# Optimization experiments

Hardware: AMD Instinct MI355X
Metric: run time of the kernel (lower is better)

Reference implementation:

```python
import jax, jax.numpy as jnp
import numpy as np

NUM_HEADS = 16
LN_EPS = 1e-5


def _rope(x):
    """lucidrains RotaryEmbedding(dim_per_head // 2): rotate only the first
    Dh//2 channels with interleaved pairs; pass the rest through.
    x: (B, H, S, Dh)"""
    S, D = x.shape[-2], x.shape[-1]
    rot = D // 2
    inv_freq = 1.0 / (10000.0 ** (jnp.arange(0, rot, 2, dtype=jnp.float32) / rot))  # (rot//2,)
    ang = jnp.arange(S, dtype=jnp.float32)[:, None] * inv_freq[None, :]             # (S, rot//2)
    ang = jnp.repeat(ang, 2, axis=-1)                                               # (S, rot)
    cos, sin = jnp.cos(ang), jnp.sin(ang)
    xr, xp = x[..., :rot], x[..., rot:]
    x1, x2 = xr[..., 0::2], xr[..., 1::2]
    rot_half = jnp.stack((-x2, x1), axis=-1).reshape(xr.shape)  # interleaved (-x2, x1)
    xr = xr * cos + rot_half * sin
    return jnp.concatenate([xr, xp], axis=-1)


def setup_inputs() -> dict:
    key = jax.random.key(0)
    k1, k2, k3 = jax.random.split(key, 3)
    B, S, D = 4, 2048, 2048
    X = jax.random.normal(k1, (B, S, D), dtype=jnp.float32)
    ln_w = jnp.ones((D,), dtype=jnp.float32)
    ln_b = jnp.zeros((D,), dtype=jnp.float32)
    W_in = jax.random.normal(k2, (D, 3 * D), dtype=jnp.float32) * 0.02
    W_out = jax.random.normal(k3, (D, D), dtype=jnp.float32) * 0.02
    return {"X": X, "ln_w": ln_w, "ln_b": ln_b, "W_in": W_in, "W_out": W_out}


def reference(X, ln_w, ln_b, W_in, W_out):
    B, S, D = X.shape
    H = NUM_HEADS
    Dh = D // H
    # pre-norm (LayerNorm)
    mu = jnp.mean(X, axis=-1, keepdims=True)
    var = jnp.mean(jnp.square(X - mu), axis=-1, keepdims=True)
    Xn = (X - mu) * jax.lax.rsqrt(var + LN_EPS) * ln_w + ln_b
    # fused QKV projection
    qkv = jnp.einsum('bsd,df->bsf', Xn, W_in)            # (B, S, 3D)
    Q, K, V = jnp.split(qkv, 3, axis=-1)
    Q = Q.reshape(B, S, H, Dh).transpose(0, 2, 1, 3)     # (B, H, S, Dh)
    K = K.reshape(B, S, H, Dh).transpose(0, 2, 1, 3)
    V = V.reshape(B, S, H, Dh).transpose(0, 2, 1, 3)
    Q, K = _rope(Q), _rope(K)
    scores = jnp.einsum('bhqd,bhkd->bhqk', Q, K) / jnp.sqrt(jnp.float32(Dh))
    probs = jax.nn.softmax(scores, axis=-1)              # acausal: no mask
    ctx = jnp.einsum('bhqk,bhkd->bhqd', probs, V)
    ctx = ctx.transpose(0, 2, 1, 3).reshape(B, S, D)
    out = jnp.einsum('bsd,df->bsf', ctx, W_out)
    return out + X
```

## Files before the change

### kernel.cpp

```cpp
#include <hip/hip_runtime.h>
#include <hip/hip_bf16.h>
#include <cstddef>

#define B_ 4
#define S_ 2048
#define D_ 2048
#define H_ 16
#define DH_ 128
#define QKS_ 4096

typedef __attribute__((ext_vector_type(8))) short bfrag8;
typedef __attribute__((ext_vector_type(4))) float ffrag4;

typedef const __attribute__((address_space(1))) void* gptr1;
typedef __attribute__((address_space(3))) void* lptr3;
#define GL16(g, l) __builtin_amdgcn_global_load_lds((gptr1)(g), (lptr3)(l), 16, 0, 0)

#define BARRIER() { asm volatile("" ::: "memory"); __builtin_amdgcn_s_barrier(); asm volatile("" ::: "memory"); }
#define VMW8() asm volatile("s_waitcnt vmcnt(8)" ::: "memory")
#define VMW4() asm volatile("s_waitcnt vmcnt(4)" ::: "memory")
#define VMW0() asm volatile("s_waitcnt vmcnt(0)" ::: "memory")

__device__ __forceinline__ short f2bf(float f) {
  unsigned u = __float_as_uint(f);
  u = (u + 0x7FFFu + ((u >> 16) & 1u)) >> 16;
  return (short)u;
}
__device__ __forceinline__ float bf2f(short s) {
  return __uint_as_float(((unsigned)(unsigned short)s) << 16);
}
__device__ __forceinline__ unsigned pk2(float lo, float hi) {
  unsigned a = __float_as_uint(lo);
  a = (a + 0x7FFFu + ((a >> 16) & 1u)) >> 16;
  unsigned b = __float_as_uint(hi);
  b = (b + 0x7FFFu + ((b >> 16) & 1u)) & 0xFFFF0000u;
  return a | b;
}

__global__ __launch_bounds__(256) void rope_tab_kernel(float2* __restrict__ tab) {
  int idx = blockIdx.x * 256 + threadIdx.x;
  int s = idx >> 5, p = idx & 31;
  float invf = exp2f(-(float)p * (13.287712379549449f / 32.0f));
  float sn, cs;
  sincosf((float)s * invf, &sn, &cs);
  tab[idx] = make_float2(cs, sn);
}

__global__ __launch_bounds__(256) void ln_kernel(const float* __restrict__ X,
    const float* __restrict__ w, const float* __restrict__ bta,
    short* __restrict__ Xn) {
  int row = blockIdx.x;
  int tid = threadIdx.x;
  const float* xr = X + (size_t)row * D_;
  float x[8];
  float4 v0 = *(const float4*)(xr + tid * 4);
  float4 v1 = *(const float4*)(xr + 1024 + tid * 4);
  x[0] = v0.x; x[1] = v0.y; x[2] = v0.z; x[3] = v0.w;
  x[4] = v1.x; x[5] = v1.y; x[6] = v1.z; x[7] = v1.w;
  float sum = 0.f, ssq = 0.f;
#pragma unroll
  for (int i = 0; i < 8; i++) { sum += x[i]; ssq += x[i] * x[i]; }
#pragma unroll
  for (int off = 1; off < 64; off <<= 1) {
    sum += __shfl_xor(sum, off, 64);
    ssq += __shfl_xor(ssq, off, 64);
  }
  __shared__ float s1[4], s2[4];
  int wave = tid >> 6;
  if ((tid & 63) == 0) { s1[wave] = sum; s2[wave] = ssq; }
  __syncthreads();
  sum = s1[0] + s1[1] + s1[2] + s1[3];
  ssq = s2[0] + s2[1] + s2[2] + s2[3];
  float mu = sum * (1.0f / D_);
  float var = ssq * (1.0f / D_) - mu * mu;
  float rs = rsqrtf(var + 1e-5f);
  short* orow = Xn + (size_t)row * D_;
#pragma unroll
  for (int i = 0; i < 8; i++) {
    int col = (i < 4) ? (tid * 4 + i) : (1024 + tid * 4 + (i - 4));
    float xn = (x[i] - mu) * rs * w[col] + bta[col];
    orow[col] = f2bf(xn);
  }
}

__global__ __launch_bounds__(256) void transpose_cvt(const float* __restrict__ W,
    short* __restrict__ WT, int R, int C) {
  __shared__ float t[32][33];
  int tx = threadIdx.x, ty = threadIdx.y;
  int c0 = blockIdx.x * 32, r0 = blockIdx.y * 32;
#pragma unroll
  for (int i = 0; i < 4; i++)
    t[ty + i * 8][tx] = W[(size_t)(r0 + ty + i * 8) * C + c0 + tx];
  __syncthreads();
#pragma unroll
  for (int i = 0; i < 4; i++)
    WT[(size_t)(c0 + ty + i * 8) * R + r0 + tx] = f2bf(t[tx][ty + i * 8]);
}

template<int EPI>
__global__ __launch_bounds__(512) void gemm_bt(const short* __restrict__ A,
    const short* __restrict__ Bt, short* __restrict__ Cb, short* __restrict__ Vt,
    const float2* __restrict__ tab, float* __restrict__ Cf,
    const float* __restrict__ resid, int M, int N, int K) {
  __shared__ __align__(16) short lA[2][2][256][32];
  __shared__ __align__(16) short lB[2][2][256][32];
  int tid = threadIdx.x;
  int wave = tid >> 6, lane = tid & 63;
  int m16 = lane & 15, quad = lane >> 4;
  int wm = (wave >> 2) * 128, wn = (wave & 3) * 64;

  int bid = blockIdx.x;
  int q = bid & 7, c = bid >> 3;
  int xb = c >> 2;
  int yb = (q << 2) | (c & 3);
  int m0 = yb * 256, n0 = xb * 256;

  const ffrag4 fzero = {0.f, 0.f, 0.f, 0.f};
  ffrag4 acc[8][4];
#pragma unroll
  for (int i = 0; i < 8; i++)
#pragma unroll
    for (int j = 0; j < 4; j++) acc[i][j] = fzero;

  int r0_ = tid >> 2;
  int csw = ((tid & 3) ^ ((r0_ >> 1) & 3)) << 3;
  const short* gA0 = A + (size_t)(m0 + r0_) * K + csw;
  const short* gA1 = A + (size_t)(m0 + r0_ + 128) * K + csw;
  const short* gB0 = Bt + (size_t)(n0 + r0_) * K + csw;
  const short* gB1 = Bt + (size_t)(n0 + r0_ + 128) * K + csw;
  int ldW = wave << 10;

#define STG(g0, g1, larr, kt, h, d) { \
    const short* s0_ = (g0) + ((size_t)(kt) << 6) + ((h) << 5); \
    const short* s1_ = (g1) + ((size_t)(kt) << 6) + ((h) << 5); \
    char* dst_ = (char*)(larr) + (((d) << 15) | ((h) << 14)) + ldW; \
    GL16(s0_, dst_); \
    GL16(s1_, dst_ + 8192); }

  int offA[8], offB[4];
#pragma unroll
  for (int mi = 0; mi < 8; mi++) {
    int ra = wm + mi * 16 + m16;
    offA[mi] = ra * 64 + ((quad ^ ((ra >> 1) & 3)) << 4);
  }
#pragma unroll
  for (int ni = 0; ni < 4; ni++) {
    int rb = wn + ni * 16 + m16;
    offB[ni] = rb * 64 + ((quad ^ ((rb >> 1) & 3)) << 4);
  }
  const char* cA = (const char*)lA;
  const char* cB = (const char*)lB;

  STG(gA0, gA1, lA, 0, 0, 0); STG(gB0, gB1, lB, 0, 0, 0);
  STG(gA0, gA1, lA, 0, 1, 0); STG(gB0, gB1, lB, 0, 1, 0);
  STG(gA0, gA1, lA, 1, 0, 1); STG(gB0, gB1, lB, 1, 0, 1);
  VMW8();
  BARRIER();

  int nK = K >> 6;
  for (int t = 0; t < nK; ++t) {
    int cur = t & 1, nxt = cur ^ 1;
    int s1 = (t + 1 < nK), s2 = (t + 2 < nK);
    int h0 = cur << 15;
    int h1 = h0 | 16384;
    bfrag8 bf[4], af[4];

#pragma unroll
    for (int ni = 0; ni < 4; ni++) bf[ni] = *(const bfrag8*)(cB + h0 + offB[ni]);
#pragma unroll
    for (int mi = 0; mi < 4; mi++) af[mi] = *(const bfrag8*)(cA + h0 + offA[mi]);
    if (s1) STG(gA0, gA1, lA, t + 1, 1, nxt);
    BARRIER();
    __builtin_amdgcn_s_setprio(1);
#pragma unroll
    for (int mi = 0; mi < 4; mi++)
#pragma unroll
      for (int ni = 0; ni < 4; ni++)
        acc[mi][ni] = __builtin_amdgcn_mfma_f32_16x16x32_bf16(af[mi], bf[ni], acc[mi][ni], 0, 0, 0);
    __builtin_amdgcn_s_setprio(0);
    BARRIER();

#pragma unroll
    for (int mi = 0; mi < 4; mi++) af[mi] = *(const bfrag8*)(cA + h0 + offA[mi + 4]);
    if (s1) STG(gB0, gB1, lB, t + 1, 1, nxt);
    BARRIER();
    __builtin_amdgcn_s_setprio(1);
#pragma unroll
    for (int mi = 0; mi < 4; mi++)
#pragma unroll
      for (int ni = 0; ni < 4; ni++)
        acc[mi + 4][ni] = __builtin_amdgcn_mfma_f32_16x16x32_bf16(af[mi], bf[ni], acc[mi + 4][ni], 0, 0, 0);
    __builtin_amdgcn_s_setprio(0);
    if (s1) { VMW8(); } else { VMW0(); }
    BARRIER();

#pragma unroll
    for (int ni = 0; ni < 4; ni++) bf[ni] = *(const bfrag8*)(cB + h1 + offB[ni]);
#pragma unroll
    for (int mi = 0; mi < 4; mi++) af[mi] = *(const bfrag8*)(cA + h1 + offA[mi]);
    if (s2) STG(gA0, gA1, lA, t + 2, 0, cur);
    BARRIER();
    __builtin_amdgcn_s_setprio(1);
#pragma unroll
    for (int mi = 0; mi < 4; mi++)
#pragma unroll
      for (int ni = 0; ni < 4; ni++)
        acc[mi][ni] = __builtin_amdgcn_mfma_f32_16x16x32_bf16(af[mi], bf[ni], acc[mi][ni], 0, 0, 0);
    __builtin_amdgcn_s_setprio(0);
    BARRIER();

#pragma unroll
    for (int mi = 0; mi < 4; mi++) af[mi] = *(const bfrag8*)(cA + h1 + offA[mi + 4]);
    if (s2) STG(gB0, gB1, lB, t + 2, 0, cur);
    BARRIER();
    __builtin_amdgcn_s_setprio(1);
#pragma unroll
    for (int mi = 0; mi < 4; mi++)
#pragma unroll
      for (int ni = 0; ni < 4; ni++)
        acc[mi + 4][ni] = __builtin_amdgcn_mfma_f32_16x16x32_bf16(af[mi], bf[ni], acc[mi + 4][ni], 0, 0, 0);
    __builtin_amdgcn_s_setprio(0);
    if (s2) { VMW8(); } else if (s1) { VMW4(); }
    BARRIER();
  }
#undef STG

#pragma unroll
  for (int mi = 0; mi < 8; mi++) {
    int rowb = m0 + wm + mi * 16 + quad * 4;
#pragma unroll
    for (int ni = 0; ni < 4; ni++) {
      int col = n0 + wn + ni * 16 + m16;
      if (EPI == 1) {
#pragma unroll
        for (int r = 0; r < 4; r++) {
          size_t idx = (size_t)(rowb + r) * N + col;
          Cf[idx] = acc[mi][ni][r] + resid[idx];
        }
      } else if (n0 >= 4096) {
        int d = col - 4096;
        short4 pk;
        pk.x = f2bf(acc[mi][ni][0]);
        pk.y = f2bf(acc[mi][ni][1]);
        pk.z = f2bf(acc[mi][ni][2]);
        pk.w = f2bf(acc[mi][ni][3]);
        *(short4*)(Vt + ((size_t)((rowb >> 11) * H_ + (d >> 7)) * DH_ + (d & 127)) * S_ +
                   (rowb & (S_ - 1))) = pk;
      } else if ((col & 127) < 64) {
        int p = (col & 127) >> 1;
        float sgn = (col & 1) ? 1.0f : -1.0f;
#pragma unroll
        for (int r = 0; r < 4; r++) {
          float own = acc[mi][ni][r];
          float prt = __shfl_xor(own, 1, 64);
          float2 cssn = tab[((rowb + r) & (S_ - 1)) * 32 + p];
          Cb[(size_t)(rowb + r) * QKS_ + col] = f2bf(own * cssn.x + sgn * prt * cssn.y);
        }
      } else {
#pragma unroll
        for (int r = 0; r < 4; r++)
          Cb[(size_t)(rowb + r) * QKS_ + col] = f2bf(acc[mi][ni][r]);
      }
    }
  }
}

__global__ __launch_bounds__(512) void attn_kernel(const short* __restrict__ qkv,
    const short* __restrict__ Vt, short* __restrict__ ctx) {
  __shared__ __align__(16) short lK[2][64 * 128];
  __shared__ __align__(16) short lV[2][128 * 64];
  int tid = threadIdx.x;
  int wave = tid >> 6, lane = tid & 63;
  int m16 = lane & 15, quad = lane >> 4;
  int bh = blockIdx.y;
  int b = bh >> 4, h = bh & 15;
  int qbase = blockIdx.x * 256 + wave * 32;

  const float qscale = 1.4426950408889634f * 0.08838834764831845f;
  bfrag8 qf[2][4];
#pragma unroll
  for (int qb = 0; qb < 2; qb++)
#pragma unroll
    for (int kc = 0; kc < 4; kc++) {
      bfrag8 q = *(const bfrag8*)(qkv +
          (size_t)(b * S_ + qbase + qb * 16 + m16) * QKS_ + h * DH_ + kc * 32 + quad * 8);
#pragma unroll
      for (int j = 0; j < 8; j++) q[j] = f2bf(bf2f(q[j]) * qscale);
      qf[qb][kc] = q;
    }

  const ffrag4 fzero = {0.f, 0.f, 0.f, 0.f};
  ffrag4 oacc[2][8];
#pragma unroll
  for (int qb = 0; qb < 2; qb++)
#pragma unroll
    for (int nd = 0; nd < 8; nd++) oacc[qb][nd] = fzero;
  float lpart[2] = {0.f, 0.f};

  int krow = lane >> 4;
  int kcb = lane & 15;
  int vrow = lane >> 3;
  int vcb = lane & 7;

  {
#pragma unroll
    for (int i = 0; i < 2; i++) {
      int c = wave + i * 8;
      int r = c * 4 + krow;
      int sb = kcb ^ (r & 15);
      GL16(qkv + (size_t)(b * S_ + r) * QKS_ + D_ + h * DH_ + sb * 8, &lK[0][c * 512]);
    }
#pragma unroll
    for (int i = 0; i < 2; i++) {
      int c = wave + i * 8;
      int r = c * 8 + vrow;
      int sb = vcb ^ (r & 7);
      GL16(Vt + (size_t)(bh * DH_ + r) * S_ + sb * 8, &lV[0][c * 512]);
    }
  }
  __syncthreads();

  for (int kt = 0; kt < 32; kt++) {
    int cur = kt & 1;
    if (kt < 31) {
      int sk0 = (kt + 1) * 64;
      int nb = cur ^ 1;
#pragma unroll
      for (int i = 0; i < 2; i++) {
        int c = wave + i * 8;
        int r = c * 4 + krow;
        int sb = kcb ^ (r & 15);
        GL16(qkv + (size_t)(b * S_ + sk0 + r) * QKS_ + D_ + h * DH_ + sb * 8, &lK[nb][c * 512]);
      }
#pragma unroll
      for (int i = 0; i < 2; i++) {
        int c = wave + i * 8;
        int r = c * 8 + vrow;
        int sb = vcb ^ (r & 7);
        GL16(Vt + (size_t)(bh * DH_ + r) * S_ + sk0 + sb * 8, &lV[nb][c * 512]);
      }
    }

    const short* kb = &lK[cur][0];
    const short* vb = &lV[cur][0];

    ffrag4 sacc[2][4];
#pragma unroll
    for (int qb = 0; qb < 2; qb++)
#pragma unroll
      for (int ntk = 0; ntk < 4; ntk++) sacc[qb][ntk] = fzero;
#pragma unroll
    for (int ntk = 0; ntk < 4; ntk++)
#pragma unroll
      for (int kc = 0; kc < 4; kc++) {
        bfrag8 kf = *(const bfrag8*)(kb + (ntk * 16 + m16) * 128 +
                                     (((kc * 4 + quad) ^ m16) << 3));
        sacc[0][ntk] = __builtin_amdgcn_mfma_f32_16x16x32_bf16(kf, qf[0][kc], sacc[0][ntk], 0, 0, 0);
        sacc[1][ntk] = __builtin_amdgcn_mfma_f32_16x16x32_bf16(kf, qf[1][kc], sacc[1][ntk], 0, 0, 0);
      }

    bfrag8 pA[2][2];
#pragma unroll
    for (int qb = 0; qb < 2; qb++) {
      unsigned Xp[4][2];
      float ls = 0.f;
#pragma unroll
      for (int ntk = 0; ntk < 4; ntk++) {
        float e0 = exp2f(sacc[qb][ntk][0]);
        float e1 = exp2f(sacc[qb][ntk][1]);
        float e2 = exp2f(sacc[qb][ntk][2]);
        float e3 = exp2f(sacc[qb][ntk][3]);
        ls += (e0 + e1) + (e2 + e3);
        Xp[ntk][0] = pk2(e0, e1);
        Xp[ntk][1] = pk2(e2, e3);
      }
      lpart[qb] += ls;
#pragma unroll
      for (int kc = 0; kc < 2; kc++) {
        unsigned x0 = Xp[2 * kc][0], x1 = Xp[2 * kc][1];
        unsigned y0 = Xp[2 * kc + 1][0], y1 = Xp[2 * kc + 1][1];
        asm("v_permlane32_swap_b32 %0, %1" : "+v"(x0), "+v"(y0));
        asm("v_permlane16_swap_b32 %0, %1" : "+v"(x0), "+v"(y0));
        asm("v_permlane32_swap_b32 %0, %1" : "+v"(x1), "+v"(y1));
        asm("v_permlane16_swap_b32 %0, %1" : "+v"(x1), "+v"(y1));
        union { int4 i4; bfrag8 b8; } u;
        u.i4 = (int4){(int)x0, (int)x1, (int)y0, (int)y1};
        pA[qb][kc] = u.b8;
      }
    }

#pragma unroll
    for (int kc = 0; kc < 2; kc++)
#pragma unroll
      for (int nd = 0; nd < 8; nd++) {
        bfrag8 vf = *(const bfrag8*)(vb + (nd * 16 + m16) * 64 +
                                     (((kc * 4 + quad) ^ (m16 & 7)) << 3));
        oacc[0][nd] = __builtin_amdgcn_mfma_f32_16x16x32_bf16(pA[0][kc], vf, oacc[0][nd], 0, 0, 0);
        oacc[1][nd] = __builtin_amdgcn_mfma_f32_16x16x32_bf16(pA[1][kc], vf, oacc[1][nd], 0, 0, 0);
      }

    __syncthreads();
  }

#pragma unroll
  for (int qb = 0; qb < 2; qb++) {
    lpart[qb] += __shfl_xor(lpart[qb], 16, 64);
    lpart[qb] += __shfl_xor(lpart[qb], 32, 64);
  }
#pragma unroll
  for (int qb = 0; qb < 2; qb++) {
    float inv[4];
#pragma unroll
    for (int r = 0; r < 4; r++) inv[r] = 1.0f / __shfl(lpart[qb], quad * 4 + r, 64);
#pragma unroll
    for (int nd = 0; nd < 8; nd++)
#pragma unroll
      for (int r = 0; r < 4; r++) {
        int row = qbase + qb * 16 + quad * 4 + r;
        int col = h * DH_ + nd * 16 + m16;
        ctx[(size_t)(b * S_ + row) * D_ + col] = f2bf(oacc[qb][nd][r] * inv[r]);
      }
  }
}

extern "C" void kernel_launch(void* const* d_in, const int* in_sizes, int n_in,
                              void* d_out, int out_size, void* d_ws, size_t ws_size,
                              hipStream_t stream) {
  const float* X    = (const float*)d_in[0];
  const float* lnw  = (const float*)d_in[1];
  const float* lnb  = (const float*)d_in[2];
  const float* Win  = (const float*)d_in[3];
  const float* Wout = (const float*)d_in[4];
  float* out = (float*)d_out;
  char* ws = (char*)d_ws;
  short*  Xn    = (short*)(ws + 0);
  short*  WinT  = (short*)(ws + 33554432);
  short*  WoutT = (short*)(ws + 58720256);
  short*  qkv   = (short*)(ws + 67108864);
  short*  Vt    = (short*)(ws + 134217728);
  short*  ctx   = (short*)(ws + 167772160);
  float2* tab   = (float2*)(ws + 201326592);

  rope_tab_kernel<<<256, 256, 0, stream>>>(tab);
  transpose_cvt<<<dim3(192, 64), dim3(32, 8), 0, stream>>>(Win, WinT, 2048, 6144);
  transpose_cvt<<<dim3(64, 64), dim3(32, 8), 0, stream>>>(Wout, WoutT, 2048, 2048);
  ln_kernel<<<8192, 256, 0, stream>>>(X, lnw, lnb, Xn);
  gemm_bt<0><<<768, 512, 0, stream>>>(Xn, WinT, qkv, Vt, tab, nullptr, nullptr, 8192, 6144, 2048);
  attn_kernel<<<dim3(8, 64), 512, 0, stream>>>(qkv, Vt, ctx);
  gemm_bt<1><<<256, 512, 0, stream>>>(ctx, WoutT, nullptr, nullptr, nullptr, out, X, 8192, 2048, 2048);
}
```

Baseline: 647.2 us.

## Software-pipeline LDS fragment loads with MFMA via double-buffered register fragments

Restructures the GEMM K-loop so LDS reads for the next sub-tile are issued while MFMAs for the current sub-tile run. Fragments are ping-ponged between two register sets, barriers drop from eight to four per K-tile, and the loop is peeled so the tail iterations need no runtime conditionals. It also adds a launch-bounds occupancy hint of two blocks and retunes the vmcnt waits. The extra fragment registers raise register pressure, which could cause spills under the tighter occupancy bound, and the reworked wait counts must still cover the async global-to-LDS copies.

```diff
diff --git a/kernel.cpp b/kernel.cpp
--- a/kernel.cpp
+++ b/kernel.cpp
@@ -18,6 +18,7 @@
 
 #define BARRIER() { asm volatile("" ::: "memory"); __builtin_amdgcn_s_barrier(); asm volatile("" ::: "memory"); }
 #define VMW8() asm volatile("s_waitcnt vmcnt(8)" ::: "memory")
+#define VMW6() asm volatile("s_waitcnt vmcnt(6)" ::: "memory")
 #define VMW4() asm volatile("s_waitcnt vmcnt(4)" ::: "memory")
 #define VMW0() asm volatile("s_waitcnt vmcnt(0)" ::: "memory")
 
@@ -98,7 +99,7 @@
 }
 
 template<int EPI>
-__global__ __launch_bounds__(512) void gemm_bt(const short* __restrict__ A,
+__global__ __launch_bounds__(512, 2) void gemm_bt(const short* __restrict__ A,
     const short* __restrict__ Bt, short* __restrict__ Cb, short* __restrict__ Vt,
     const float2* __restrict__ tab, float* __restrict__ Cf,
     const float* __restrict__ resid, int M, int N, int K) {
@@ -151,78 +152,89 @@
   const char* cA = (const char*)lA;
   const char* cB = (const char*)lB;
 
+  bfrag8 afA[4], afB[4], bfA[4], bfB[4];
+
+#define MF16(AF, BF, BASE) { \
+    __builtin_amdgcn_s_setprio(1); \
+    _Pragma("unroll") \
+    for (int mi_ = 0; mi_ < 4; mi_++) \
+      _Pragma("unroll") \
+      for (int ni_ = 0; ni_ < 4; ni_++) \
+        acc[(BASE) + mi_][ni_] = __builtin_amdgcn_mfma_f32_16x16x32_bf16( \
+            AF[mi_], BF[ni_], acc[(BASE) + mi_][ni_], 0, 0, 0); \
+    __builtin_amdgcn_s_setprio(0); }
+
+#define KTILE(T, S1, S2) { \
+    const int cur_ = (T) & 1, nxt_ = cur_ ^ 1; \
+    const int h0_ = cur_ << 15; \
+    const int h1_ = h0_ | 16384; \
+    const int g0_ = nxt_ << 15; \
+     \
+    BARRIER(); \
+    afB[0] = *(const bfrag8*)(cA + h0_ + offA[4]); \
+    afB[1] = *(const bfrag8*)(cA + h0_ + offA[5]); \
+    afB[2] = *(const bfrag8*)(cA + h0_ + offA[6]); \
+    afB[3] = *(const bfrag8*)(cA + h0_ + offA[7]); \
+    if (S1) STG(gA0, gA1, lA, (T) + 1, 1, nxt_); \
+    MF16(afA, bfA, 0); \
+    if (S1) { VMW6(); } else { VMW0(); } \
+     \
+    BARRIER(); \
+    bfB[0] = *(const bfrag8*)(cB + h1_ + offB[0]); \
+    bfB[1] = *(const bfrag8*)(cB + h1_ + offB[1]); \
+    bfB[2] = *(const bfrag8*)(cB + h1_ + offB[2]); \
+    bfB[3] = *(const bfrag8*)(cB + h1_ + offB[3]); \
+    afA[0] = *(const bfrag8*)(cA + h1_ + offA[0]); \
+    afA[1] = *(const bfrag8*)(cA + h1_ + offA[1]); \
+    afA[2] = *(const bfrag8*)(cA + h1_ + offA[2]); \
+    afA[3] = *(const bfrag8*)(cA + h1_ + offA[3]); \
+    if (S1) STG(gB0, gB1, lB, (T) + 1, 1, nxt_); \
+    MF16(afB, bfA, 4); \
+     \
+    BARRIER(); \
+    afB[0] = *(const bfrag8*)(cA + h1_ + offA[4]); \
+    afB[1] = *(const bfrag8*)(cA + h1_ + offA[5]); \
+    afB[2] = *(const bfrag8*)(cA + h1_ + offA[6]); \
+    afB[3] = *(const bfrag8*)(cA + h1_ + offA[7]); \
+    if (S2) STG(gA0, gA1, lA, (T) + 2, 0, cur_); \
+    MF16(afA, bfB, 0); \
+    if (S2) { VMW6(); } else if (S1) { VMW4(); } \
+     \
+    BARRIER(); \
+    if (S1) { \
+      bfA[0] = *(const bfrag8*)(cB + g0_ + offB[0]); \
+      bfA[1] = *(const bfrag8*)(cB + g0_ + offB[1]); \
+      bfA[2] = *(const bfrag8*)(cB + g0_ + offB[2]); \
+      bfA[3] = *(const bfrag8*)(cB + g0_ + offB[3]); \
+      afA[0] = *(const bfrag8*)(cA + g0_ + offA[0]); \
+      afA[1] = *(const bfrag8*)(cA + g0_ + offA[1]); \
+      afA[2] = *(const bfrag8*)(cA + g0_ + offA[2]); \
+      afA[3] = *(const bfrag8*)(cA + g0_ + offA[3]); \
+    } \
+    if (S2) STG(gB0, gB1, lB, (T) + 2, 0, cur_); \
+    MF16(afB, bfB, 4); \
+  }
+
   STG(gA0, gA1, lA, 0, 0, 0); STG(gB0, gB1, lB, 0, 0, 0);
   STG(gA0, gA1, lA, 0, 1, 0); STG(gB0, gB1, lB, 0, 1, 0);
   STG(gA0, gA1, lA, 1, 0, 1); STG(gB0, gB1, lB, 1, 0, 1);
   VMW8();
   BARRIER();
+  bfA[0] = *(const bfrag8*)(cB + offB[0]);
+  bfA[1] = *(const bfrag8*)(cB + offB[1]);
+  bfA[2] = *(const bfrag8*)(cB + offB[2]);
+  bfA[3] = *(const bfrag8*)(cB + offB[3]);
+  afA[0] = *(const bfrag8*)(cA + offA[0]);
+  afA[1] = *(const bfrag8*)(cA + offA[1]);
+  afA[2] = *(const bfrag8*)(cA + offA[2]);
+  afA[3] = *(const bfrag8*)(cA + offA[3]);
 
   int nK = K >> 6;
-  for (int t = 0; t < nK; ++t) {
-    int cur = t & 1, nxt = cur ^ 1;
-    int s1 = (t + 1 < nK), s2 = (t + 2 < nK);
-    int h0 = cur << 15;
-    int h1 = h0 | 16384;
-    bfrag8 bf[4], af[4];
-
-#pragma unroll
-    for (int ni = 0; ni < 4; ni++) bf[ni] = *(const bfrag8*)(cB + h0 + offB[ni]);
-#pragma unroll
-    for (int mi = 0; mi < 4; mi++) af[mi] = *(const bfrag8*)(cA + h0 + offA[mi]);
-    if (s1) STG(gA0, gA1, lA, t + 1, 1, nxt);
-    BARRIER();
-    __builtin_amdgcn_s_setprio(1);
-#pragma unroll
-    for (int mi = 0; mi < 4; mi++)
-#pragma unroll
-      for (int ni = 0; ni < 4; ni++)
-        acc[mi][ni] = __builtin_amdgcn_mfma_f32_16x16x32_bf16(af[mi], bf[ni], acc[mi][ni], 0, 0, 0);
-    __builtin_amdgcn_s_setprio(0);
-    BARRIER();
-
-#pragma unroll
-    for (int mi = 0; mi < 4; mi++) af[mi] = *(const bfrag8*)(cA + h0 + offA[mi + 4]);
-    if (s1) STG(gB0, gB1, lB, t + 1, 1, nxt);
-    BARRIER();
-    __builtin_amdgcn_s_setprio(1);
-#pragma unroll
-    for (int mi = 0; mi < 4; mi++)
-#pragma unroll
-      for (int ni = 0; ni < 4; ni++)
-        acc[mi + 4][ni] = __builtin_amdgcn_mfma_f32_16x16x32_bf16(af[mi], bf[ni], acc[mi + 4][ni], 0, 0, 0);
-    __builtin_amdgcn_s_setprio(0);
-    if (s1) { VMW8(); } else { VMW0(); }
-    BARRIER();
-
-#pragma unroll
-    for (int ni = 0; ni < 4; ni++) bf[ni] = *(const bfrag8*)(cB + h1 + offB[ni]);
-#pragma unroll
-    for (int mi = 0; mi < 4; mi++) af[mi] = *(const bfrag8*)(cA + h1 + offA[mi]);
-    if (s2) STG(gA0, gA1, lA, t + 2, 0, cur);
-    BARRIER();
-    __builtin_amdgcn_s_setprio(1);
-#pragma unroll
-    for (int mi = 0; mi < 4; mi++)
-#pragma unroll
-      for (int ni = 0; ni < 4; ni++)
-        acc[mi][ni] = __builtin_amdgcn_mfma_f32_16x16x32_bf16(af[mi], bf[ni], acc[mi][ni], 0, 0, 0);
-    __builtin_amdgcn_s_setprio(0);
-    BARRIER();
-
-#pragma unroll
-    for (int mi = 0; mi < 4; mi++) af[mi] = *(const bfrag8*)(cA + h1 + offA[mi + 4]);
-    if (s2) STG(gB0, gB1, lB, t + 2, 0, cur);
-    BARRIER();
-    __builtin_amdgcn_s_setprio(1);
-#pragma unroll
-    for (int mi = 0; mi < 4; mi++)
-#pragma unroll
-      for (int ni = 0; ni < 4; ni++)
-        acc[mi + 4][ni] = __builtin_amdgcn_mfma_f32_16x16x32_bf16(af[mi], bf[ni], acc[mi + 4][ni], 0, 0, 0);
-    __builtin_amdgcn_s_setprio(0);
-    if (s2) { VMW8(); } else if (s1) { VMW4(); }
-    BARRIER();
-  }
+  for (int t = 0; t < nK - 2; ++t) KTILE(t, 1, 1);
+  KTILE(nK - 2, 1, 0);
+  KTILE(nK - 1, 0, 0);
+#undef KTILE
+#undef MF16
 #undef STG
 
 #pragma unroll
```

Measured after the change: 640.9 us. About the same (-1.0%).
